# Performance work log

Measured on AMD Instinct MI355X. Metric: run time of the kernel, lower is better.

The kernel has to match this reference:

```python
import jax, jax.numpy as jnp
import numpy as np

NUM_NODES = 100000
NUM_EDGES = 1600000
DIM = 64
NUM_LAYERS = 3


def setup_inputs() -> dict:
    key = jax.random.key(0)
    k1, k2 = jax.random.split(key)
    x = jax.random.normal(k1, (NUM_NODES, DIM), dtype=jnp.float32)
    adj_t = jax.random.randint(k2, (2, NUM_EDGES), 0, NUM_NODES, dtype=jnp.int64)
    return {"x": x, "adj_t": adj_t}


def reference(x, adj_t):
    n = x.shape[0]
    # undirected -> add reversed edges (adj_t_is_undirected=True path)
    edge_index = jnp.concatenate([adj_t, adj_t[::-1]], axis=1)  # [2, 2E]
    row, col = edge_index[0], edge_index[1]
    edge_weight = jnp.ones((row.shape[0],), dtype=x.dtype)
    # gcn_norm: D^-0.5 A D^-0.5 (degree computed by scatter over col)
    deg = jax.ops.segment_sum(edge_weight, col, num_segments=n)
    deg_inv_sqrt = jnp.where(deg > 0, jax.lax.rsqrt(deg), 0.0).astype(x.dtype)
    w = deg_inv_sqrt[row] * edge_weight * deg_inv_sqrt[col]  # [2E]
    outs = [x]
    for _ in range(NUM_LAYERS):
        # gather -> scale -> scatter_add (SpMM)
        msgs = w[:, None] * x[row]                     # [2E, D]
        x = jax.ops.segment_sum(msgs, col, num_segments=n)  # [N, D]
        outs.append(x)
    return jnp.mean(jnp.stack(outs), axis=0)
```

## Files before the change

### kernel.cpp

```cpp
#include <hip/hip_runtime.h>

#define DIM 64
#define BKT_SHIFT 7
#define BKT_G 128
#define NBLK 256
#define HIST_B 1024
#define NREP 4
#define CAP 4608
#define RCAP 18

__device__ inline float blo(unsigned p) { return __uint_as_float(p << 16); }
__device__ inline float bhi(unsigned p) { return __uint_as_float(p & 0xffff0000u); }
__device__ inline unsigned bpack(float x, float y) {
    unsigned ux = __float_as_uint(x);
    unsigned uy = __float_as_uint(y);
    ux += 0x7fffu + ((ux >> 16) & 1u);
    uy += 0x7fffu + ((uy >> 16) & 1u);
    return (ux >> 16) | (uy & 0xffff0000u);
}

__global__ void zero_kernel(int* __restrict__ p, int n) {
    int i = blockIdx.x * blockDim.x + threadIdx.x;
    if (i < n) p[i] = 0;
}

__global__ __launch_bounds__(HIST_B)
void place_direct_kernel(const int* __restrict__ adj, int E,
                         int* __restrict__ gcnt,
                         unsigned* __restrict__ pairs, int NB) {
    extern __shared__ int lds[];
    int* lh  = lds;
    int* cur = lds + NREP * NB;
    for (int g = threadIdx.x; g < (NREP + 1) * NB; g += blockDim.x) lds[g] = 0;
    __syncthreads();
    const int rep = (threadIdx.x & (NREP - 1)) * NB;
    const int n4 = E >> 2;
    const int4* srcs = (const int4*)adj;
    const int4* dsts = (const int4*)(adj + E);

    int4 a0 = {0,0,0,0}, b0 = a0, a1 = a0, b1 = a0;
    int have = 0;
    for (int i = blockIdx.x * blockDim.x + threadIdx.x; i < n4;
         i += NBLK * blockDim.x) {
        int4 a = srcs[i];
        int4 b = dsts[i];
        atomicAdd(&lh[rep + (a.x >> BKT_SHIFT)], 1);
        atomicAdd(&lh[rep + (a.y >> BKT_SHIFT)], 1);
        atomicAdd(&lh[rep + (a.z >> BKT_SHIFT)], 1);
        atomicAdd(&lh[rep + (a.w >> BKT_SHIFT)], 1);
        atomicAdd(&lh[rep + (b.x >> BKT_SHIFT)], 1);
        atomicAdd(&lh[rep + (b.y >> BKT_SHIFT)], 1);
        atomicAdd(&lh[rep + (b.z >> BKT_SHIFT)], 1);
        atomicAdd(&lh[rep + (b.w >> BKT_SHIFT)], 1);
        if (have == 0)      { a0 = a; b0 = b; have = 1; }
        else if (have == 1) { a1 = a; b1 = b; have = 2; }
    }
    int te = 0, ta = 0, tb = 0;
    if (blockIdx.x == 0) {
        for (int e = (n4 << 2) + threadIdx.x; e < E; e += blockDim.x) {
            int a = adj[e];
            int b = adj[E + e];
            atomicAdd(&lh[rep + (a >> BKT_SHIFT)], 1);
            atomicAdd(&lh[rep + (b >> BKT_SHIFT)], 1);
            if (te == 0) { ta = a; tb = b; te = 1; }
        }
    }
    __syncthreads();
    for (int g = threadIdx.x; g < NB; g += blockDim.x) {
        int tot = lh[g] + lh[NB + g] + lh[2 * NB + g] + lh[3 * NB + g];
        cur[g] = (tot > 0) ? atomicAdd(&gcnt[g], tot) : 0;
    }
    __syncthreads();
#define PLACE_EMIT(av, bv)                                                     \
    {                                                                          \
        int gb = (bv) >> BKT_SHIFT;                                            \
        int p = atomicAdd(&cur[gb], 1);                                        \
        if (p < CAP)                                                           \
            pairs[(size_t)gb * CAP + p] =                                      \
                ((unsigned)((bv) & (BKT_G - 1)) << 17) | (unsigned)(av);       \
        int ga = (av) >> BKT_SHIFT;                                            \
        p = atomicAdd(&cur[ga], 1);                                            \
        if (p < CAP)                                                           \
            pairs[(size_t)ga * CAP + p] =                                      \
                ((unsigned)((av) & (BKT_G - 1)) << 17) | (unsigned)(bv);       \
    }
    if (have >= 1) {
        PLACE_EMIT(a0.x, b0.x); PLACE_EMIT(a0.y, b0.y);
        PLACE_EMIT(a0.z, b0.z); PLACE_EMIT(a0.w, b0.w);
    }
    if (have >= 2) {
        PLACE_EMIT(a1.x, b1.x); PLACE_EMIT(a1.y, b1.y);
        PLACE_EMIT(a1.z, b1.z); PLACE_EMIT(a1.w, b1.w);
    }
    {
        int it = 0;
        for (int i = blockIdx.x * blockDim.x + threadIdx.x; i < n4;
             i += NBLK * blockDim.x) {
            if (it >= 2) {
                int4 a = srcs[i];
                int4 b = dsts[i];
                PLACE_EMIT(a.x, b.x); PLACE_EMIT(a.y, b.y);
                PLACE_EMIT(a.z, b.z); PLACE_EMIT(a.w, b.w);
            }
            ++it;
        }
    }
    if (blockIdx.x == 0) {
        int tl = 0;
        for (int e = (n4 << 2) + threadIdx.x; e < E; e += blockDim.x) {
            if (tl == 0 && te == 1) {
                PLACE_EMIT(ta, tb);
            } else {
                int a = adj[e];
                int b = adj[E + e];
                PLACE_EMIT(a, b);
            }
            ++tl;
        }
    }
#undef PLACE_EMIT
}

__global__ __launch_bounds__(256)
void pass2_build_kernel(const unsigned* __restrict__ pairs,
                        const int* __restrict__ gcnt,
                        const float4* __restrict__ x,
                        int* __restrict__ csr_src,
                        int* __restrict__ row_ptr,
                        int* __restrict__ deg,
                        float* __restrict__ dinv,
                        uint4* __restrict__ xs0,
                        int N, int NB, int total_adj) {
    __shared__ int cnt[BKT_G];
    __shared__ int pre[BKT_G];
    __shared__ int cur[BKT_G];
    __shared__ float dv[BKT_G];
    __shared__ int win[CAP];
    __shared__ int red[256];
    int g = blockIdx.x;
    int base = g << BKT_SHIFT;
    size_t poff = (size_t)g * CAP;
    int m = gcnt[g];
    if (m > CAP) m = CAP;
    int lsum = 0;
    for (int h = threadIdx.x; h < g; h += 256) lsum += gcnt[h];
    red[threadIdx.x] = lsum;
    if (threadIdx.x < BKT_G) cnt[threadIdx.x] = 0;
    __syncthreads();
    for (int o = 128; o > 0; o >>= 1) {
        if (threadIdx.x < o) red[threadIdx.x] += red[threadIdx.x + o];
        __syncthreads();
    }
    int coff = red[0];
    unsigned rec[RCAP];
#pragma unroll
    for (int k = 0; k < RCAP; ++k) {
        int i = threadIdx.x + k * 256;
        unsigned p = 0;
        if (i < m) {
            p = pairs[poff + i];
            atomicAdd(&cnt[p >> 17], 1);
        }
        rec[k] = p;
    }
    __syncthreads();
    if (threadIdx.x < BKT_G) pre[threadIdx.x] = cnt[threadIdx.x];
    __syncthreads();
    for (int o = 1; o < BKT_G; o <<= 1) {
        int t = 0;
        if (threadIdx.x < BKT_G && threadIdx.x >= o) t = pre[threadIdx.x - o];
        __syncthreads();
        if (threadIdx.x < BKT_G) pre[threadIdx.x] += t;
        __syncthreads();
    }
    if (threadIdx.x < BKT_G) {
        int v = base + threadIdx.x;
        if (v < N) {
            int c = cnt[threadIdx.x];
            int lstart = pre[threadIdx.x] - c;
            float di = (c > 0) ? rsqrtf((float)c) : 0.0f;
            row_ptr[v] = coff + lstart;
            deg[v] = c;
            dinv[v] = di;
            dv[threadIdx.x] = di;
            cur[threadIdx.x] = lstart;
        }
    }
    if (g == NB - 1 && threadIdx.x == 0) row_ptr[N] = total_adj;
    __syncthreads();
#pragma unroll
    for (int k = 0; k < RCAP; ++k) {
        int i = threadIdx.x + k * 256;
        if (i < m) {
            unsigned p = rec[k];
            int pos = atomicAdd(&cur[p >> 17], 1);
            win[pos] = (int)(p & 0x1ffffu);
        }
    }
    __syncthreads();
    for (int i = threadIdx.x; i < m; i += 256)
        csr_src[coff + i] = win[i];
    for (int w = threadIdx.x; w < BKT_G * 8; w += blockDim.x) {
        int vl = w >> 3, sub = w & 7;
        int v = base + vl;
        if (v < N) {
            float di = dv[vl];
            float4 xa = x[(size_t)v * 16 + sub * 2];
            float4 xb = x[(size_t)v * 16 + sub * 2 + 1];
            uint4 o;
            o.x = bpack(di * xa.x, di * xa.y);
            o.y = bpack(di * xa.z, di * xa.w);
            o.z = bpack(di * xb.x, di * xb.y);
            o.w = bpack(di * xb.z, di * xb.w);
            xs0[(size_t)v * 8 + sub] = o;
        }
    }
}

#define SPMM_ACCUM_BODY                                                        \
    int half = threadIdx.x & 31;                                               \
    int nb = half >> 3, sub = half & 7;                                        \
    int beg = row_ptr[v];                                                      \
    int end = row_ptr[v + 1];                                                  \
    int full = (end - beg) >> 4;                                               \
    float a0 = 0, a1 = 0, a2 = 0, a3 = 0, a4 = 0, a5 = 0, a6 = 0, a7 = 0;      \
    int j = beg;                                                               \
    int s0 = 0, s1 = 0, s2 = 0, s3 = 0;                                        \
    if (full > 0) {                                                            \
        int b = j + 4 * nb;                                                    \
        s0 = csr_src[b];     s1 = csr_src[b + 1];                              \
        s2 = csr_src[b + 2]; s3 = csr_src[b + 3];                              \
    }                                                                          \
    for (int it = 0; it < full; ++it) {                                        \
        int jn = j + 16;                                                       \
        int t0 = 0, t1 = 0, t2 = 0, t3 = 0;                                    \
        if (it + 1 < full) {                                                   \
            int b = jn + 4 * nb;                                               \
            t0 = csr_src[b];     t1 = csr_src[b + 1];                          \
            t2 = csr_src[b + 2]; t3 = csr_src[b + 3];                          \
        }                                                                      \
        uint4 p0 = xs_in[(size_t)s0 * 8 + sub];                                \
        uint4 p1 = xs_in[(size_t)s1 * 8 + sub];                                \
        uint4 p2 = xs_in[(size_t)s2 * 8 + sub];                                \
        uint4 p3 = xs_in[(size_t)s3 * 8 + sub];                                \
        a0 += (blo(p0.x) + blo(p1.x)) + (blo(p2.x) + blo(p3.x));               \
        a1 += (bhi(p0.x) + bhi(p1.x)) + (bhi(p2.x) + bhi(p3.x));               \
        a2 += (blo(p0.y) + blo(p1.y)) + (blo(p2.y) + blo(p3.y));               \
        a3 += (bhi(p0.y) + bhi(p1.y)) + (bhi(p2.y) + bhi(p3.y));               \
        a4 += (blo(p0.z) + blo(p1.z)) + (blo(p2.z) + blo(p3.z));               \
        a5 += (bhi(p0.z) + bhi(p1.z)) + (bhi(p2.z) + bhi(p3.z));               \
        a6 += (blo(p0.w) + blo(p1.w)) + (blo(p2.w) + blo(p3.w));               \
        a7 += (bhi(p0.w) + bhi(p1.w)) + (bhi(p2.w) + bhi(p3.w));               \
        s0 = t0; s1 = t1; s2 = t2; s3 = t3;                                    \
        j = jn;                                                                \
    }                                                                          \
    for (int idx = j + nb; idx < end; idx += 4) {                              \
        int s = csr_src[idx];                                                  \
        uint4 p = xs_in[(size_t)s * 8 + sub];                                  \
        a0 += blo(p.x); a1 += bhi(p.x);                                        \
        a2 += blo(p.y); a3 += bhi(p.y);                                        \
        a4 += blo(p.z); a5 += bhi(p.z);                                        \
        a6 += blo(p.w); a7 += bhi(p.w);                                        \
    }                                                                          \
    a0 += __shfl_xor(a0, 8);  a0 += __shfl_xor(a0, 16);                        \
    a1 += __shfl_xor(a1, 8);  a1 += __shfl_xor(a1, 16);                        \
    a2 += __shfl_xor(a2, 8);  a2 += __shfl_xor(a2, 16);                        \
    a3 += __shfl_xor(a3, 8);  a3 += __shfl_xor(a3, 16);                        \
    a4 += __shfl_xor(a4, 8);  a4 += __shfl_xor(a4, 16);                        \
    a5 += __shfl_xor(a5, 8);  a5 += __shfl_xor(a5, 16);                        \
    a6 += __shfl_xor(a6, 8);  a6 += __shfl_xor(a6, 16);                        \
    a7 += __shfl_xor(a7, 8);  a7 += __shfl_xor(a7, 16);

__global__ void spmm_bf16_kernel(const int* __restrict__ row_ptr,
                                 const int* __restrict__ csr_src,
                                 const float* __restrict__ dinv,
                                 const uint4* __restrict__ xs_in,
                                 uint4* __restrict__ xs_out, int N) {
    int t = blockIdx.x * blockDim.x + threadIdx.x;
    int v = t >> 5;
    if (v >= N) return;
    SPMM_ACCUM_BODY
    if (nb == 0) {
        float di = dinv[v];
        float d2 = di * di;
        uint4 o;
        o.x = bpack(d2 * a0, d2 * a1);
        o.y = bpack(d2 * a2, d2 * a3);
        o.z = bpack(d2 * a4, d2 * a5);
        o.w = bpack(d2 * a6, d2 * a7);
        xs_out[(size_t)v * 8 + sub] = o;
    }
}

__global__ void spmm_last_kernel(const int* __restrict__ row_ptr,
                                 const int* __restrict__ csr_src,
                                 const float* __restrict__ dinv,
                                 const int* __restrict__ deg,
                                 const uint4* __restrict__ xs_in,
                                 const uint4* __restrict__ xs1,
                                 const float4* __restrict__ x,
                                 float4* __restrict__ out, int N) {
    int t = blockIdx.x * blockDim.x + threadIdx.x;
    int v = t >> 5;
    if (v >= N) return;
    SPMM_ACCUM_BODY
    if (nb == 0) {
        float di = dinv[v];
        float rs = sqrtf((float)deg[v]);
        size_t idx = (size_t)v * 8 + sub;
        uint4 q1 = xs1[idx];
        uint4 q2 = xs_in[idx];
        float4 xa = x[(size_t)v * 16 + sub * 2];
        float4 xb = x[(size_t)v * 16 + sub * 2 + 1];
        float4 oa, ob;
        oa.x = 0.25f * (xa.x + rs * (blo(q1.x) + blo(q2.x)) + di * a0);
        oa.y = 0.25f * (xa.y + rs * (bhi(q1.x) + bhi(q2.x)) + di * a1);
        oa.z = 0.25f * (xa.z + rs * (blo(q1.y) + blo(q2.y)) + di * a2);
        oa.w = 0.25f * (xa.w + rs * (bhi(q1.y) + bhi(q2.y)) + di * a3);
        ob.x = 0.25f * (xb.x + rs * (blo(q1.z) + blo(q2.z)) + di * a4);
        ob.y = 0.25f * (xb.y + rs * (bhi(q1.z) + bhi(q2.z)) + di * a5);
        ob.z = 0.25f * (xb.z + rs * (blo(q1.w) + blo(q2.w)) + di * a6);
        ob.w = 0.25f * (xb.w + rs * (bhi(q1.w) + bhi(q2.w)) + di * a7);
        out[(size_t)v * 16 + sub * 2]     = oa;
        out[(size_t)v * 16 + sub * 2 + 1] = ob;
    }
}

extern "C" void kernel_launch(void* const* d_in, const int* in_sizes, int n_in,
                              void* d_out, int out_size, void* d_ws, size_t ws_size,
                              hipStream_t stream) {
    const float* x = (const float*)d_in[0];
    const int* adj = (const int*)d_in[1];
    float* out     = (float*)d_out;

    const int total_adj = in_sizes[1];
    const int E = total_adj / 2;
    const int N = in_sizes[0] / DIM;
    const int NB = (N + BKT_G - 1) / BKT_G;

    size_t BUF = (size_t)total_adj * 4;
    size_t xsb = (size_t)N * 32 * 4;
    if (xsb > BUF) BUF = xsb;
    BUF = (BUF + 255) & ~(size_t)255;
    size_t PAIRS_B = ((size_t)NB * CAP * 4 + 255) & ~(size_t)255;

    char* ws = (char*)d_ws;
    int*      deg     = (int*)(ws);
    float*    dinv    = (float*)(ws + (size_t)512 * 1024);
    int*      row_ptr = (int*)(ws + (size_t)1024 * 1024);
    int*      gcnt    = (int*)(ws + (size_t)1536 * 1024);
    char*     big     = ws + (size_t)1664 * 1024;
    int*      csr_src = (int*)(big);
    unsigned* pairs   = (unsigned*)(big + BUF);
    uint4*    xs0     = (uint4*)(big + BUF + PAIRS_B);
    uint4*    xs1     = (uint4*)(big + BUF + PAIRS_B + BUF);
    uint4*    xs2     = (uint4*)(big + BUF + PAIRS_B + 2 * BUF);

    const int B = 256;

    zero_kernel<<<(NB + 1023) / 1024, 1024, 0, stream>>>(gcnt, NB);

    place_direct_kernel<<<NBLK, HIST_B, (NREP + 1) * NB * sizeof(int), stream>>>(
        adj, E, gcnt, pairs, NB);

    pass2_build_kernel<<<NB, B, 0, stream>>>(pairs, gcnt, (const float4*)x,
                                             csr_src, row_ptr, deg, dinv,
                                             xs0, N, NB, total_adj);

    const int nblocks32 = (int)(((long long)N * 32 + B - 1) / B);
    spmm_bf16_kernel<<<nblocks32, B, 0, stream>>>(row_ptr, csr_src, dinv, xs0, xs1, N);
    spmm_bf16_kernel<<<nblocks32, B, 0, stream>>>(row_ptr, csr_src, dinv, xs1, xs2, N);
    spmm_last_kernel<<<nblocks32, B, 0, stream>>>(row_ptr, csr_src, dinv, deg,
                                                  xs2, xs1, (const float4*)x,
                                                  (float4*)out, N);
}
```

Measured before the change: 279.7 us.

## Stage bucketed edge pairs in LDS per round before global scatter

The edge-placement kernel now works in rounds. Each block builds a local bucket histogram, prefix-sums it across waves, and stages the packed pairs in shared memory sorted by bucket. It then writes them to global memory in bucket-contiguous runs, locating each entry's bucket by binary search. This replaces random per-pair global stores, and the second read of the adjacency, with grouped writes and a single read. The cost is more barriers, per-round global atomics on the bucket counters, and the binary-search overhead.

```diff
diff --git a/kernel.cpp b/kernel.cpp
--- a/kernel.cpp
+++ b/kernel.cpp
@@ -5,7 +5,7 @@
 #define BKT_G 128
 #define NBLK 256
 #define HIST_B 1024
-#define NREP 4
+#define SCAP (HIST_B * 8)
 #define CAP 4608
 #define RCAP 18
 
@@ -28,97 +28,113 @@
 void place_direct_kernel(const int* __restrict__ adj, int E,
                          int* __restrict__ gcnt,
                          unsigned* __restrict__ pairs, int NB) {
-    extern __shared__ int lds[];
-    int* lh  = lds;
-    int* cur = lds + NREP * NB;
-    for (int g = threadIdx.x; g < (NREP + 1) * NB; g += blockDim.x) lds[g] = 0;
-    __syncthreads();
-    const int rep = (threadIdx.x & (NREP - 1)) * NB;
+    extern __shared__ int L[];
+    int* cnt    = L;
+    int* lb     = L + NB;
+    int* cur    = L + 2 * NB + 1;
+    int* gb     = L + 3 * NB + 1;
+    int* wsum   = L + 4 * NB + 1;
+    int* staged = L + 4 * NB + 17;
+    const int tid  = threadIdx.x;
+    const int lane = tid & 63;
+    const int wid  = tid >> 6;
     const int n4 = E >> 2;
     const int4* srcs = (const int4*)adj;
     const int4* dsts = (const int4*)(adj + E);
-
-    int4 a0 = {0,0,0,0}, b0 = a0, a1 = a0, b1 = a0;
-    int have = 0;
-    for (int i = blockIdx.x * blockDim.x + threadIdx.x; i < n4;
-         i += NBLK * blockDim.x) {
-        int4 a = srcs[i];
-        int4 b = dsts[i];
-        atomicAdd(&lh[rep + (a.x >> BKT_SHIFT)], 1);
-        atomicAdd(&lh[rep + (a.y >> BKT_SHIFT)], 1);
-        atomicAdd(&lh[rep + (a.z >> BKT_SHIFT)], 1);
-        atomicAdd(&lh[rep + (a.w >> BKT_SHIFT)], 1);
-        atomicAdd(&lh[rep + (b.x >> BKT_SHIFT)], 1);
-        atomicAdd(&lh[rep + (b.y >> BKT_SHIFT)], 1);
-        atomicAdd(&lh[rep + (b.z >> BKT_SHIFT)], 1);
-        atomicAdd(&lh[rep + (b.w >> BKT_SHIFT)], 1);
-        if (have == 0)      { a0 = a; b0 = b; have = 1; }
-        else if (have == 1) { a1 = a; b1 = b; have = 2; }
-    }
-    int te = 0, ta = 0, tb = 0;
+    const int nrounds = (n4 + NBLK * HIST_B - 1) / (NBLK * HIST_B);
+
+    for (int r = 0; r < nrounds; ++r) {
+        for (int g = tid; g < NB; g += HIST_B) cnt[g] = 0;
+        __syncthreads();
+        int i = (r * NBLK + blockIdx.x) * HIST_B + tid;
+        int4 a = {0, 0, 0, 0}, b = {0, 0, 0, 0};
+        int valid = 0;
+        if (i < n4) {
+            a = srcs[i];
+            b = dsts[i];
+            valid = 1;
+            atomicAdd(&cnt[a.x >> BKT_SHIFT], 1);
+            atomicAdd(&cnt[a.y >> BKT_SHIFT], 1);
+            atomicAdd(&cnt[a.z >> BKT_SHIFT], 1);
+            atomicAdd(&cnt[a.w >> BKT_SHIFT], 1);
+            atomicAdd(&cnt[b.x >> BKT_SHIFT], 1);
+            atomicAdd(&cnt[b.y >> BKT_SHIFT], 1);
+            atomicAdd(&cnt[b.z >> BKT_SHIFT], 1);
+            atomicAdd(&cnt[b.w >> BKT_SHIFT], 1);
+        }
+        __syncthreads();
+        int v = (tid < NB) ? cnt[tid] : 0;
+        int s = v;
+#pragma unroll
+        for (int off = 1; off < 64; off <<= 1) {
+            int o = __shfl_up(s, off);
+            if (lane >= off) s += o;
+        }
+        if (lane == 63) wsum[wid] = s;
+        __syncthreads();
+        if (wid == 0 && lane < 16) {
+            int w = wsum[lane];
+#pragma unroll
+            for (int off = 1; off < 16; off <<= 1) {
+                int o = __shfl_up(w, off);
+                if (lane >= off) w += o;
+            }
+            wsum[lane] = w;
+        }
+        __syncthreads();
+        int incl = s + (wid ? wsum[wid - 1] : 0);
+        if (tid < NB) {
+            lb[tid + 1] = incl;
+            cur[tid] = incl - v;
+            gb[tid]  = (v > 0) ? atomicAdd(&gcnt[tid], v) : 0;
+        }
+        if (tid == 0) lb[0] = 0;
+        __syncthreads();
+        int total = lb[NB];
+        if (valid) {
+#define STAGE_EMIT(av, bv)                                                     \
+    {                                                                          \
+        int g_ = (bv) >> BKT_SHIFT;                                            \
+        int p_ = atomicAdd(&cur[g_], 1);                                       \
+        staged[p_] = (int)(((unsigned)((bv) & (BKT_G - 1)) << 17) |            \
+                           (unsigned)(av));                                    \
+        g_ = (av) >> BKT_SHIFT;                                                \
+        p_ = atomicAdd(&cur[g_], 1);                                           \
+        staged[p_] = (int)(((unsigned)((av) & (BKT_G - 1)) << 17) |            \
+                           (unsigned)(bv));                                    \
+    }
+            STAGE_EMIT(a.x, b.x); STAGE_EMIT(a.y, b.y);
+            STAGE_EMIT(a.z, b.z); STAGE_EMIT(a.w, b.w);
+#undef STAGE_EMIT
+        }
+        __syncthreads();
+        for (int k = tid; k < total; k += HIST_B) {
+            int lo = 0, hi = NB - 1;
+            while (lo < hi) {
+                int mid = (lo + hi + 1) >> 1;
+                if (lb[mid] <= k) lo = mid; else hi = mid - 1;
+            }
+            int p = gb[lo] + (k - lb[lo]);
+            if (p < CAP)
+                pairs[(size_t)lo * CAP + p] = (unsigned)staged[k];
+        }
+        __syncthreads();
+    }
     if (blockIdx.x == 0) {
-        for (int e = (n4 << 2) + threadIdx.x; e < E; e += blockDim.x) {
-            int a = adj[e];
-            int b = adj[E + e];
-            atomicAdd(&lh[rep + (a >> BKT_SHIFT)], 1);
-            atomicAdd(&lh[rep + (b >> BKT_SHIFT)], 1);
-            if (te == 0) { ta = a; tb = b; te = 1; }
-        }
-    }
-    __syncthreads();
-    for (int g = threadIdx.x; g < NB; g += blockDim.x) {
-        int tot = lh[g] + lh[NB + g] + lh[2 * NB + g] + lh[3 * NB + g];
-        cur[g] = (tot > 0) ? atomicAdd(&gcnt[g], tot) : 0;
-    }
-    __syncthreads();
-#define PLACE_EMIT(av, bv)                                                     \
-    {                                                                          \
-        int gb = (bv) >> BKT_SHIFT;                                            \
-        int p = atomicAdd(&cur[gb], 1);                                        \
-        if (p < CAP)                                                           \
-            pairs[(size_t)gb * CAP + p] =                                      \
-                ((unsigned)((bv) & (BKT_G - 1)) << 17) | (unsigned)(av);       \
-        int ga = (av) >> BKT_SHIFT;                                            \
-        p = atomicAdd(&cur[ga], 1);                                            \
-        if (p < CAP)                                                           \
-            pairs[(size_t)ga * CAP + p] =                                      \
-                ((unsigned)((av) & (BKT_G - 1)) << 17) | (unsigned)(bv);       \
-    }
-    if (have >= 1) {
-        PLACE_EMIT(a0.x, b0.x); PLACE_EMIT(a0.y, b0.y);
-        PLACE_EMIT(a0.z, b0.z); PLACE_EMIT(a0.w, b0.w);
-    }
-    if (have >= 2) {
-        PLACE_EMIT(a1.x, b1.x); PLACE_EMIT(a1.y, b1.y);
-        PLACE_EMIT(a1.z, b1.z); PLACE_EMIT(a1.w, b1.w);
-    }
-    {
-        int it = 0;
-        for (int i = blockIdx.x * blockDim.x + threadIdx.x; i < n4;
-             i += NBLK * blockDim.x) {
-            if (it >= 2) {
-                int4 a = srcs[i];
-                int4 b = dsts[i];
-                PLACE_EMIT(a.x, b.x); PLACE_EMIT(a.y, b.y);
-                PLACE_EMIT(a.z, b.z); PLACE_EMIT(a.w, b.w);
-            }
-            ++it;
-        }
-    }
-    if (blockIdx.x == 0) {
-        int tl = 0;
-        for (int e = (n4 << 2) + threadIdx.x; e < E; e += blockDim.x) {
-            if (tl == 0 && te == 1) {
-                PLACE_EMIT(ta, tb);
-            } else {
-                int a = adj[e];
-                int b = adj[E + e];
-                PLACE_EMIT(a, b);
-            }
-            ++tl;
-        }
-    }
-#undef PLACE_EMIT
+        for (int e = (n4 << 2) + tid; e < E; e += HIST_B) {
+            int av = adj[e], bv = adj[E + e];
+            int g1 = bv >> BKT_SHIFT;
+            int p1 = atomicAdd(&gcnt[g1], 1);
+            if (p1 < CAP)
+                pairs[(size_t)g1 * CAP + p1] =
+                    ((unsigned)(bv & (BKT_G - 1)) << 17) | (unsigned)av;
+            int g2 = av >> BKT_SHIFT;
+            int p2 = atomicAdd(&gcnt[g2], 1);
+            if (p2 < CAP)
+                pairs[(size_t)g2 * CAP + p2] =
+                    ((unsigned)(av & (BKT_G - 1)) << 17) | (unsigned)bv;
+        }
+    }
 }
 
 __global__ __launch_bounds__(256)
@@ -360,8 +376,9 @@
 
     zero_kernel<<<(NB + 1023) / 1024, 1024, 0, stream>>>(gcnt, NB);
 
-    place_direct_kernel<<<NBLK, HIST_B, (NREP + 1) * NB * sizeof(int), stream>>>(
-        adj, E, gcnt, pairs, NB);
+    size_t place_lds = (size_t)(4 * NB + 17 + SCAP) * sizeof(int);
+    place_direct_kernel<<<NBLK, HIST_B, place_lds, stream>>>(adj, E, gcnt,
+                                                             pairs, NB);
 
     pass2_build_kernel<<<NB, B, 0, stream>>>(pairs, gcnt, (const float4*)x,
                                              csr_src, row_ptr, deg, dinv,
```

Measured after the change: 280.2 us, median of 2. No clear change (+0.2%).
